# Performance work log

Measured on AMD Instinct MI355X. Metric: run time of the kernel, lower is better.

Reference implementation:

```python
import jax, jax.numpy as jnp
import numpy as np

B, H, W, C = 4, 64, 64, 256
C8 = C // 8

def setup_inputs() -> dict:
    key = jax.random.key(0)
    k1, k2, k3, k4 = jax.random.split(key, 4)
    # glorot-uniform-ish init for 1x1 conv kernels stored as [Cin, Cout]
    def glorot(k, cin, cout):
        lim = np.sqrt(6.0 / (cin + cout)).astype(np.float32)
        return jax.random.uniform(k, (cin, cout), jnp.float32, -lim, lim)
    return {
        "x": jax.random.normal(k1, (B, H, W, C), jnp.float32),
        "kernel_f": glorot(k2, C, C8),
        "kernel_g": glorot(k3, C, C8),
        "kernel_h": glorot(k4, C, C),
        "gamma": jnp.zeros((1,), jnp.float32),
    }

def reference(x, kernel_f, kernel_g, kernel_h, gamma):
    b, h, w, c = x.shape
    n = h * w
    xf = x.reshape(b, n, c)                       # [B, N, C]
    # 1x1 convs == per-position matmuls
    f = jnp.einsum('bnc,cd->bnd', xf, kernel_f)   # [B, N, C/8]
    g = jnp.einsum('bnc,cd->bnd', xf, kernel_g)   # [B, N, C/8]
    hh = jnp.einsum('bnc,cd->bnd', xf, kernel_h)  # [B, N, C]
    s = jnp.einsum('bnd,bmd->bnm', g, f)          # [B, N, N]
    beta = jax.nn.softmax(s, axis=-1)
    o = jnp.einsum('bnm,bmc->bnc', beta, hh)      # [B, N, C]
    o = o.reshape(b, h, w, c)
    return gamma * o + x
```

## Files before the change

### kernel.cpp

```cpp
#include <hip/hip_runtime.h>
#include <hip/hip_bf16.h>

typedef __bf16 bf16x8 __attribute__((ext_vector_type(8)));
typedef float f32x4 __attribute__((ext_vector_type(4)));
typedef float f32x16 __attribute__((ext_vector_type(16)));
typedef unsigned short u16;
typedef unsigned int u32;

__device__ __forceinline__ u16 f2bf_rne(float f){
  union { float f; u32 u; } v; v.f = f;
  u32 r = v.u + 0x7fffu + ((v.u >> 16) & 1u);
  return (u16)(r >> 16);
}
__device__ __forceinline__ u32 pack2(float a, float b){
  return __builtin_amdgcn_perm(__float_as_uint(a), __float_as_uint(b), 0x03020706u);
}
#define BARRIER_LGKM() asm volatile("s_waitcnt lgkmcnt(0)\n\ts_barrier" ::: "memory")

__global__ __launch_bounds__(512) void prep_kernel(
    const float* __restrict__ Wf, const float* __restrict__ Wg,
    const float* __restrict__ Wh, u16* __restrict__ Wfrag){
  const int cc = blockIdx.x;
  const int t = threadIdx.x;
  const int kk = t >> 6, lane = t & 63;
  const int L = lane & 15, quad = lane >> 4;
  const int n = cc * 16 + L;
  u32 pk[4];
  #pragma unroll
  for (int j2 = 0; j2 < 4; ++j2){
    float v[2];
    #pragma unroll
    for (int h = 0; h < 2; ++h){
      int k = kk * 32 + quad * 8 + j2 * 2 + h;
      if (n < 256)      v[h] = Wh[k * 256 + n];
      else if (n < 288) v[h] = Wf[k * 32 + (n - 256)];
      else              v[h] = Wg[k * 32 + (n - 288)];
    }
    pk[j2] = (u32)f2bf_rne(v[0]) | ((u32)f2bf_rne(v[1]) << 16);
  }
  uint4* dst = (uint4*)(Wfrag + ((size_t)(cc * 8 + kk) * 64 + lane) * 8);
  *dst = make_uint4(pk[0], pk[1], pk[2], pk[3]);
}

__global__ __launch_bounds__(512) void proj_kernel(
    const float* __restrict__ x, const u16* __restrict__ Wfrag,
    u16* __restrict__ Qg, u16* __restrict__ Kg, u16* __restrict__ Vfrag)
{
  __shared__ __align__(16) u16 smem[256 * 72];
  u16 (*xb)[264] = (u16(*)[264])smem;
  u16 (*Vr)[72]  = (u16(*)[72])smem;

  const int tid = threadIdx.x;
  const int lane = tid & 63, wave = tid >> 6;
  const int L = lane & 15, quad = lane >> 4;
  const int rowgrp = wave >> 1, colhalf = wave & 1;
  const int n0 = blockIdx.x * 64;

  const float4* xsrc = (const float4*)(x + (size_t)n0 * 256);
  #pragma unroll
  for (int j = 0; j < 8; ++j){
    int idx = j * 512 + tid;
    int row = idx >> 6, col4 = idx & 63;
    float4 v = xsrc[idx];
    u32 p0 = (u32)f2bf_rne(v.x) | ((u32)f2bf_rne(v.y) << 16);
    u32 p1 = (u32)f2bf_rne(v.z) | ((u32)f2bf_rne(v.w) << 16);
    *(uint2*)&xb[row][col4 * 4] = make_uint2(p0, p1);
  }
  __syncthreads();

  f32x4 acc[10];
  #pragma unroll
  for (int cc = 0; cc < 10; ++cc) acc[cc] = (f32x4){0.f, 0.f, 0.f, 0.f};

  #pragma unroll
  for (int kk = 0; kk < 8; ++kk){
    bf16x8 a = *(const bf16x8*)&xb[rowgrp * 16 + L][kk * 32 + quad * 8];
    #pragma unroll
    for (int cc = 0; cc < 10; ++cc){
      int ccg = colhalf * 10 + cc;
      bf16x8 bfr = *(const bf16x8*)(Wfrag + ((size_t)(ccg * 8 + kk) * 64 + lane) * 8);
      acc[cc] = __builtin_amdgcn_mfma_f32_16x16x32_bf16(a, bfr, acc[cc], 0, 0, 0);
    }
  }

  if (colhalf){
    #pragma unroll
    for (int cc = 6; cc < 10; ++cc){
      int ccg = 10 + cc;
      u16* dst = (ccg < 18) ? Kg : Qg;
      float sc = (ccg < 18) ? 1.0f : 1.44269504088896f;
      int c = (ccg & 1) * 16 + L;
      #pragma unroll
      for (int r = 0; r < 4; ++r){
        int row = n0 + rowgrp * 16 + quad * 4 + r;
        dst[(size_t)row * 32 + c] = f2bf_rne(acc[cc][r] * sc);
      }
    }
  }

  __syncthreads();

  {
    const int cmax = colhalf ? 6 : 10;
    for (int cc = 0; cc < cmax; ++cc){
      int ccg = colhalf * 10 + cc;
      int c = ccg * 16 + L;
      #pragma unroll
      for (int r = 0; r < 4; ++r){
        int tn = rowgrp * 16 + quad * 4 + r;
        int p  = ((tn & 15) << 2) | (tn >> 4);
        Vr[c][p] = f2bf_rne(acc[cc][r]);
      }
    }
  }
  __syncthreads();

  u16* Vblk = Vfrag + (size_t)blockIdx.x * (256 * 64);
  #pragma unroll
  for (int i = 0; i < 4; ++i){
    int idx = i * 512 + tid;
    *(uint4*)(Vblk + (size_t)idx * 8) = *(const uint4*)&Vr[idx & 255][(idx >> 8) * 8];
  }
}

__global__ __launch_bounds__(512) void flash_kernel(
    const u16* __restrict__ Qg, const u16* __restrict__ Kg, const u16* __restrict__ Vfrag,
    const float* __restrict__ x, const float* __restrict__ gamma, float* __restrict__ out)
{
  constexpr float SH = -92.33248261689366f;
  __shared__ __align__(16) char smem[73728];
  u16 (*Plds)[2][2][64][72] = (u16 (*)[2][2][64][72])smem;
  float (*Osh)[256] = (float (*)[256])smem;
  __shared__ float Lsh[2][64];

  const int tid = threadIdx.x, lane = tid & 63, wave = tid >> 6;
  const int L = lane & 15, quad = lane >> 4;
  const int m32 = lane & 31, h32 = lane >> 5;
  const int half = wave >> 2, wv = wave & 3;

  const int id = blockIdx.x;
  const int xcd = id & 7;
  const int b = xcd >> 1;
  const int qt = (xcd & 1) * 32 + (id >> 3);
  const int q0 = qt * 64;

  const u16* Qb = Qg + (size_t)(b * 4096) * 32;
  const u16* Kb = Kg + (size_t)(b * 4096) * 32;
  const u16* Vb = Vfrag + (size_t)b * (64 * 256 * 64);
  const float gm = gamma[0];

  const int g0 = half * 32;

  bf16x8 qa = *(const bf16x8*)(Qb + (size_t)(q0 + wv * 16 + L) * 32 + quad * 8);

  const u16* kpA = Kb + (size_t)(g0 * 64 + L) * 32 + quad * 8;
  bf16x8 kcA0 = *(const bf16x8*)(kpA);
  bf16x8 kcA1 = *(const bf16x8*)(kpA + 512);
  bf16x8 kcA2 = *(const bf16x8*)(kpA + 1024);
  bf16x8 kcA3 = *(const bf16x8*)(kpA + 1536);
  const u16* kpB = kpA + 2048;
  bf16x8 kcB0 = *(const bf16x8*)(kpB);
  bf16x8 kcB1 = *(const bf16x8*)(kpB + 512);
  bf16x8 kcB2 = *(const bf16x8*)(kpB + 1024);
  bf16x8 kcB3 = *(const bf16x8*)(kpB + 1536);

  bf16x8 vfA[8], vfB[8];
  {
    const u16* Vt = Vb + (size_t)g0 * (256 * 64);
    #pragma unroll
    for (int ks = 0; ks < 4; ++ks){
      const u16* vrow = Vt + (size_t)((ks * 2 + h32) * 256 + wv * 64 + m32) * 8;
      vfA[ks * 2]     = *(const bf16x8*)(vrow);
      vfA[ks * 2 + 1] = *(const bf16x8*)(vrow + 32 * 8);
      vfB[ks * 2]     = *(const bf16x8*)(vrow + 16384);
      vfB[ks * 2 + 1] = *(const bf16x8*)(vrow + 16384 + 32 * 8);
    }
  }

  f32x16 acc[4];
  #pragma unroll
  for (int t = 0; t < 4; ++t)
    #pragma unroll
    for (int i = 0; i < 16; ++i) acc[t][i] = 0.f;
  float lsum[4] = {0.f, 0.f, 0.f, 0.f};
  const f32x4 zero = (f32x4){0.f, 0.f, 0.f, 0.f};

  for (int it = 0; it < 16; ++it){
    const int g = g0 + it * 2;
    u16 (*PwA)[72] = Plds[half][it & 1][0];
    u16 (*PwB)[72] = Plds[half][it & 1][1];

    f32x4 sA0 = __builtin_amdgcn_mfma_f32_16x16x32_bf16(qa, kcA0, zero, 0, 0, 0);
    f32x4 sA1 = __builtin_amdgcn_mfma_f32_16x16x32_bf16(qa, kcA1, zero, 0, 0, 0);
    f32x4 sA2 = __builtin_amdgcn_mfma_f32_16x16x32_bf16(qa, kcA2, zero, 0, 0, 0);
    f32x4 sA3 = __builtin_amdgcn_mfma_f32_16x16x32_bf16(qa, kcA3, zero, 0, 0, 0);
    f32x4 sB0 = __builtin_amdgcn_mfma_f32_16x16x32_bf16(qa, kcB0, zero, 0, 0, 0);
    f32x4 sB1 = __builtin_amdgcn_mfma_f32_16x16x32_bf16(qa, kcB1, zero, 0, 0, 0);
    f32x4 sB2 = __builtin_amdgcn_mfma_f32_16x16x32_bf16(qa, kcB2, zero, 0, 0, 0);
    f32x4 sB3 = __builtin_amdgcn_mfma_f32_16x16x32_bf16(qa, kcB3, zero, 0, 0, 0);

    if (it < 15){
      const u16* kpa = Kb + (size_t)((g + 2) * 64 + L) * 32 + quad * 8;
      kcA0 = *(const bf16x8*)(kpa);
      kcA1 = *(const bf16x8*)(kpa + 512);
      kcA2 = *(const bf16x8*)(kpa + 1024);
      kcA3 = *(const bf16x8*)(kpa + 1536);
      const u16* kpb = kpa + 2048;
      kcB0 = *(const bf16x8*)(kpb);
      kcB1 = *(const bf16x8*)(kpb + 512);
      kcB2 = *(const bf16x8*)(kpb + 1024);
      kcB3 = *(const bf16x8*)(kpb + 1536);
    }

    #pragma unroll
    for (int r = 0; r < 4; ++r){
      float a0 = __builtin_amdgcn_exp2f(sA0[r] + SH);
      float a1 = __builtin_amdgcn_exp2f(sA1[r] + SH);
      float a2 = __builtin_amdgcn_exp2f(sA2[r] + SH);
      float a3 = __builtin_amdgcn_exp2f(sA3[r] + SH);
      float b0 = __builtin_amdgcn_exp2f(sB0[r] + SH);
      float b1 = __builtin_amdgcn_exp2f(sB1[r] + SH);
      float b2 = __builtin_amdgcn_exp2f(sB2[r] + SH);
      float b3 = __builtin_amdgcn_exp2f(sB3[r] + SH);
      lsum[r] += ((a0 + a1) + (a2 + a3)) + ((b0 + b1) + (b2 + b3));
      *(uint2*)&PwA[wv * 16 + quad * 4 + r][L * 4] =
          make_uint2(pack2(a0, a1), pack2(a2, a3));
      *(uint2*)&PwB[wv * 16 + quad * 4 + r][L * 4] =
          make_uint2(pack2(b0, b1), pack2(b2, b3));
    }

    BARRIER_LGKM();

    #pragma unroll
    for (int ks = 0; ks < 4; ++ks){
      bf16x8 af0 = *(const bf16x8*)&PwA[m32][ks * 16 + h32 * 8];
      bf16x8 af1 = *(const bf16x8*)&PwA[32 + m32][ks * 16 + h32 * 8];
      acc[0] = __builtin_amdgcn_mfma_f32_32x32x16_bf16(af0, vfA[ks*2],   acc[0], 0, 0, 0);
      acc[1] = __builtin_amdgcn_mfma_f32_32x32x16_bf16(af0, vfA[ks*2+1], acc[1], 0, 0, 0);
      acc[2] = __builtin_amdgcn_mfma_f32_32x32x16_bf16(af1, vfA[ks*2],   acc[2], 0, 0, 0);
      acc[3] = __builtin_amdgcn_mfma_f32_32x32x16_bf16(af1, vfA[ks*2+1], acc[3], 0, 0, 0);
    }
    #pragma unroll
    for (int ks = 0; ks < 4; ++ks){
      bf16x8 af0 = *(const bf16x8*)&PwB[m32][ks * 16 + h32 * 8];
      bf16x8 af1 = *(const bf16x8*)&PwB[32 + m32][ks * 16 + h32 * 8];
      acc[0] = __builtin_amdgcn_mfma_f32_32x32x16_bf16(af0, vfB[ks*2],   acc[0], 0, 0, 0);
      acc[1] = __builtin_amdgcn_mfma_f32_32x32x16_bf16(af0, vfB[ks*2+1], acc[1], 0, 0, 0);
      acc[2] = __builtin_amdgcn_mfma_f32_32x32x16_bf16(af1, vfB[ks*2],   acc[2], 0, 0, 0);
      acc[3] = __builtin_amdgcn_mfma_f32_32x32x16_bf16(af1, vfB[ks*2+1], acc[3], 0, 0, 0);
    }

    if (it < 15){
      const u16* Vn = Vb + (size_t)(g + 2) * (256 * 64);
      #pragma unroll
      for (int ks = 0; ks < 4; ++ks){
        const u16* vrow = Vn + (size_t)((ks * 2 + h32) * 256 + wv * 64 + m32) * 8;
        vfA[ks * 2]     = *(const bf16x8*)(vrow);
        vfA[ks * 2 + 1] = *(const bf16x8*)(vrow + 32 * 8);
        vfB[ks * 2]     = *(const bf16x8*)(vrow + 16384);
        vfB[ks * 2 + 1] = *(const bf16x8*)(vrow + 16384 + 32 * 8);
      }
    }
  }

  BARRIER_LGKM();

  #pragma unroll
  for (int r = 0; r < 4; ++r){
    lsum[r] += __shfl_xor(lsum[r], 1);
    lsum[r] += __shfl_xor(lsum[r], 2);
    lsum[r] += __shfl_xor(lsum[r], 4);
    lsum[r] += __shfl_xor(lsum[r], 8);
  }
  if (L == 0){
    #pragma unroll
    for (int r = 0; r < 4; ++r) Lsh[half][wv * 16 + quad * 4 + r] = lsum[r];
  }
  if (half == 1){
    #pragma unroll
    for (int t = 0; t < 4; ++t){
      const int qi = t >> 1, ci = t & 1;
      #pragma unroll
      for (int rg = 0; rg < 16; ++rg){
        int row = qi * 32 + (rg & 3) + 8 * (rg >> 2) + 4 * h32;
        Osh[row][wv * 64 + ci * 32 + m32] = acc[t][rg];
      }
    }
  }
  __syncthreads();
  if (wave == 0){
    float li = gm / (Lsh[0][lane] + Lsh[1][lane]);
    Lsh[0][lane] = li;
  }
  __syncthreads();
  if (half == 0){
    #pragma unroll
    for (int t = 0; t < 4; ++t){
      const int qi = t >> 1, ci = t & 1;
      #pragma unroll
      for (int rg = 0; rg < 16; ++rg){
        int row = qi * 32 + (rg & 3) + 8 * (rg >> 2) + 4 * h32;
        int col = wv * 64 + ci * 32 + m32;
        Osh[row][col] = (acc[t][rg] + Osh[row][col]) * Lsh[0][row];
      }
    }
  }
  __syncthreads();
  const size_t base = ((size_t)(b * 4096) + q0) * 256;
  const float4* xs = (const float4*)(x + base);
  float4* od = (float4*)(out + base);
  const float4* Of = (const float4*)&Osh[0][0];
  #pragma unroll
  for (int i = 0; i < 8; ++i){
    int idx = i * 512 + tid;
    float4 o = Of[idx], xv = xs[idx];
    o.x += xv.x; o.y += xv.y; o.z += xv.z; o.w += xv.w;
    od[idx] = o;
  }
}

extern "C" void kernel_launch(void* const* d_in, const int* in_sizes, int n_in,
                              void* d_out, int out_size, void* d_ws, size_t ws_size,
                              hipStream_t stream) {
  const float* x     = (const float*)d_in[0];
  const float* Wf    = (const float*)d_in[1];
  const float* Wg    = (const float*)d_in[2];
  const float* Wh    = (const float*)d_in[3];
  const float* gamma = (const float*)d_in[4];
  float* out = (float*)d_out;

  u16* p = (u16*)d_ws;
  u16* Qg    = p;  p += 16384 * 32;
  u16* Kg    = p;  p += 16384 * 32;
  u16* Vfrag = p;  p += 4 * 64 * 256 * 64;
  u16* Wfrag = p;  p += 20 * 8 * 64 * 8;

  prep_kernel<<<20, 512, 0, stream>>>(Wf, Wg, Wh, Wfrag);
  proj_kernel<<<256, 512, 0, stream>>>(x, Wfrag, Qg, Kg, Vfrag);
  flash_kernel<<<256, 512, 0, stream>>>(Qg, Kg, Vfrag, x, gamma, out);
}
```

Baseline: 151.7 us.

## Stage K tiles through LDS via async global_load_lds in MFMA fragment layout

```diff
diff --git a/kernel.cpp b/kernel.cpp
--- a/kernel.cpp
+++ b/kernel.cpp
@@ -14,6 +14,10 @@
 }
 __device__ __forceinline__ u32 pack2(float a, float b){
   return __builtin_amdgcn_perm(__float_as_uint(a), __float_as_uint(b), 0x03020706u);
+}
+__device__ __forceinline__ void load_lds16(const void* g, void* l){
+  __builtin_amdgcn_global_load_lds((const __attribute__((address_space(1))) void*)g,
+                                   (__attribute__((address_space(3))) void*)l, 16, 0, 0);
 }
 #define BARRIER_LGKM() asm volatile("s_waitcnt lgkmcnt(0)\n\ts_barrier" ::: "memory")
 
@@ -44,7 +48,7 @@
 
 __global__ __launch_bounds__(512) void proj_kernel(
     const float* __restrict__ x, const u16* __restrict__ Wfrag,
-    u16* __restrict__ Qg, u16* __restrict__ Kg, u16* __restrict__ Vfrag)
+    u16* __restrict__ Qg, u16* __restrict__ Kfrag, u16* __restrict__ Vfrag)
 {
   __shared__ __align__(16) u16 smem[256 * 72];
   u16 (*xb)[264] = (u16(*)[264])smem;
@@ -87,13 +91,17 @@
     #pragma unroll
     for (int cc = 6; cc < 10; ++cc){
       int ccg = 10 + cc;
-      u16* dst = (ccg < 18) ? Kg : Qg;
-      float sc = (ccg < 18) ? 1.0f : 1.44269504088896f;
       int c = (ccg & 1) * 16 + L;
       #pragma unroll
       for (int r = 0; r < 4; ++r){
         int row = n0 + rowgrp * 16 + quad * 4 + r;
-        dst[(size_t)row * 32 + c] = f2bf_rne(acc[cc][r] * sc);
+        if (ccg < 18){
+          size_t off = ((size_t)(row >> 6) * 4 + ((row >> 4) & 3)) * 512
+                     + (c >> 3) * 128 + (row & 15) * 8 + (c & 7);
+          Kfrag[off] = f2bf_rne(acc[cc][r]);
+        } else {
+          Qg[(size_t)row * 32 + c] = f2bf_rne(acc[cc][r] * 1.44269504088896f);
+        }
       }
     }
   }
@@ -124,13 +132,14 @@
 }
 
 __global__ __launch_bounds__(512) void flash_kernel(
-    const u16* __restrict__ Qg, const u16* __restrict__ Kg, const u16* __restrict__ Vfrag,
+    const u16* __restrict__ Qg, const u16* __restrict__ Kfrag, const u16* __restrict__ Vfrag,
     const float* __restrict__ x, const float* __restrict__ gamma, float* __restrict__ out)
 {
   constexpr float SH = -92.33248261689366f;
   __shared__ __align__(16) char smem[73728];
   u16 (*Plds)[2][2][64][72] = (u16 (*)[2][2][64][72])smem;
   float (*Osh)[256] = (float (*)[256])smem;
+  __shared__ __align__(16) u16 Kl[2][2][8][512];
   __shared__ float Lsh[2][64];
 
   const int tid = threadIdx.x, lane = tid & 63, wave = tid >> 6;
@@ -145,25 +154,24 @@
   const int q0 = qt * 64;
 
   const u16* Qb = Qg + (size_t)(b * 4096) * 32;
-  const u16* Kb = Kg + (size_t)(b * 4096) * 32;
+  const u16* Kb = Kfrag + (size_t)b * 131072;
   const u16* Vb = Vfrag + (size_t)b * (64 * 256 * 64);
   const float gm = gamma[0];
 
   const int g0 = half * 32;
+  const int c0 = wv * 2;
 
   bf16x8 qa = *(const bf16x8*)(Qb + (size_t)(q0 + wv * 16 + L) * 32 + quad * 8);
-
-  const u16* kpA = Kb + (size_t)(g0 * 64 + L) * 32 + quad * 8;
-  bf16x8 kcA0 = *(const bf16x8*)(kpA);
-  bf16x8 kcA1 = *(const bf16x8*)(kpA + 512);
-  bf16x8 kcA2 = *(const bf16x8*)(kpA + 1024);
-  bf16x8 kcA3 = *(const bf16x8*)(kpA + 1536);
-  const u16* kpB = kpA + 2048;
-  bf16x8 kcB0 = *(const bf16x8*)(kpB);
-  bf16x8 kcB1 = *(const bf16x8*)(kpB + 512);
-  bf16x8 kcB2 = *(const bf16x8*)(kpB + 1024);
-  bf16x8 kcB3 = *(const bf16x8*)(kpB + 1536);
-
+  asm volatile("" ::: "memory");
+  {
+    const u16* s0 = Kb + ((size_t)(g0 + 0) * 4 + c0) * 512 + lane * 8;
+    load_lds16(s0,       &Kl[half][0][c0][0]);
+    load_lds16(s0 + 512, &Kl[half][0][c0 + 1][0]);
+    const u16* s1 = Kb + ((size_t)(g0 + 2) * 4 + c0) * 512 + lane * 8;
+    load_lds16(s1,       &Kl[half][1][c0][0]);
+    load_lds16(s1 + 512, &Kl[half][1][c0 + 1][0]);
+  }
+  asm volatile("" ::: "memory");
   bf16x8 vfA[8], vfB[8];
   {
     const u16* Vt = Vb + (size_t)g0 * (256 * 64);
@@ -176,6 +184,19 @@
       vfB[ks * 2 + 1] = *(const bf16x8*)(vrow + 16384 + 32 * 8);
     }
   }
+  asm volatile("s_waitcnt vmcnt(18)" ::: "memory");
+  bf16x8 kcA0, kcA1, kcA2, kcA3, kcB0, kcB1, kcB2, kcB3;
+  {
+    const u16 (*Ks)[512] = Kl[half][0];
+    kcA0 = *(const bf16x8*)&Ks[0][lane * 8];
+    kcA1 = *(const bf16x8*)&Ks[1][lane * 8];
+    kcA2 = *(const bf16x8*)&Ks[2][lane * 8];
+    kcA3 = *(const bf16x8*)&Ks[3][lane * 8];
+    kcB0 = *(const bf16x8*)&Ks[4][lane * 8];
+    kcB1 = *(const bf16x8*)&Ks[5][lane * 8];
+    kcB2 = *(const bf16x8*)&Ks[6][lane * 8];
+    kcB3 = *(const bf16x8*)&Ks[7][lane * 8];
+  }
 
   f32x16 acc[4];
   #pragma unroll
@@ -186,7 +207,6 @@
   const f32x4 zero = (f32x4){0.f, 0.f, 0.f, 0.f};
 
   for (int it = 0; it < 16; ++it){
-    const int g = g0 + it * 2;
     u16 (*PwA)[72] = Plds[half][it & 1][0];
     u16 (*PwB)[72] = Plds[half][it & 1][1];
 
@@ -198,19 +218,6 @@
     f32x4 sB1 = __builtin_amdgcn_mfma_f32_16x16x32_bf16(qa, kcB1, zero, 0, 0, 0);
     f32x4 sB2 = __builtin_amdgcn_mfma_f32_16x16x32_bf16(qa, kcB2, zero, 0, 0, 0);
     f32x4 sB3 = __builtin_amdgcn_mfma_f32_16x16x32_bf16(qa, kcB3, zero, 0, 0, 0);
-
-    if (it < 15){
-      const u16* kpa = Kb + (size_t)((g + 2) * 64 + L) * 32 + quad * 8;
-      kcA0 = *(const bf16x8*)(kpa);
-      kcA1 = *(const bf16x8*)(kpa + 512);
-      kcA2 = *(const bf16x8*)(kpa + 1024);
-      kcA3 = *(const bf16x8*)(kpa + 1536);
-      const u16* kpb = kpa + 2048;
-      kcB0 = *(const bf16x8*)(kpb);
-      kcB1 = *(const bf16x8*)(kpb + 512);
-      kcB2 = *(const bf16x8*)(kpb + 1024);
-      kcB3 = *(const bf16x8*)(kpb + 1536);
-    }
 
     #pragma unroll
     for (int r = 0; r < 4; ++r){
@@ -231,6 +238,27 @@
 
     BARRIER_LGKM();
 
+    {
+      int pp = (it + 2) & 15;
+      const u16* ks = Kb + ((size_t)(g0 + pp * 2) * 4 + c0) * 512 + lane * 8;
+      load_lds16(ks,       &Kl[half][it & 1][c0][0]);
+      load_lds16(ks + 512, &Kl[half][it & 1][c0 + 1][0]);
+    }
+    asm volatile("" ::: "memory");
+
+    if (it < 15){
+      asm volatile("s_waitcnt vmcnt(18)" ::: "memory");
+      const u16 (*Ks)[512] = Kl[half][(it + 1) & 1];
+      kcA0 = *(const bf16x8*)&Ks[0][lane * 8];
+      kcA1 = *(const bf16x8*)&Ks[1][lane * 8];
+      kcA2 = *(const bf16x8*)&Ks[2][lane * 8];
+      kcA3 = *(const bf16x8*)&Ks[3][lane * 8];
+      kcB0 = *(const bf16x8*)&Ks[4][lane * 8];
+      kcB1 = *(const bf16x8*)&Ks[5][lane * 8];
+      kcB2 = *(const bf16x8*)&Ks[6][lane * 8];
+      kcB3 = *(const bf16x8*)&Ks[7][lane * 8];
+    }
+
     #pragma unroll
     for (int ks = 0; ks < 4; ++ks){
       bf16x8 af0 = *(const bf16x8*)&PwA[m32][ks * 16 + h32 * 8];
@@ -251,7 +279,7 @@
     }
 
     if (it < 15){
-      const u16* Vn = Vb + (size_t)(g + 2) * (256 * 64);
+      const u16* Vn = Vb + (size_t)(g0 + (it + 1) * 2) * (256 * 64);
       #pragma unroll
       for (int ks = 0; ks < 4; ++ks){
         const u16* vrow = Vn + (size_t)((ks * 2 + h32) * 256 + wv * 64 + m32) * 8;
@@ -331,11 +359,11 @@
 
   u16* p = (u16*)d_ws;
   u16* Qg    = p;  p += 16384 * 32;
-  u16* Kg    = p;  p += 16384 * 32;
+  u16* Kfrag = p;  p += 256 * 4 * 64 * 8;
   u16* Vfrag = p;  p += 4 * 64 * 256 * 64;
   u16* Wfrag = p;  p += 20 * 8 * 64 * 8;
 
   prep_kernel<<<20, 512, 0, stream>>>(Wf, Wg, Wh, Wfrag);
-  proj_kernel<<<256, 512, 0, stream>>>(x, Wfrag, Qg, Kg, Vfrag);
-  flash_kernel<<<256, 512, 0, stream>>>(Qg, Kg, Vfrag, x, gamma, out);
-}
+  proj_kernel<<<256, 512, 0, stream>>>(x, Wfrag, Qg, Kfrag, Vfrag);
+  flash_kernel<<<256, 512, 0, stream>>>(Qg, Kfrag, Vfrag, x, gamma, out);
+}
```

After: 153.0 us. About the same (+0.9%).

## Warp-specialize flash kernel into QK/softmax producer and PV consumer waves

Applied to the files above, without the earlier changes.

```diff
diff --git a/kernel.cpp b/kernel.cpp
--- a/kernel.cpp
+++ b/kernel.cpp
@@ -128,15 +128,16 @@
     const float* __restrict__ x, const float* __restrict__ gamma, float* __restrict__ out)
 {
   constexpr float SH = -92.33248261689366f;
-  __shared__ __align__(16) char smem[73728];
-  u16 (*Plds)[2][2][64][72] = (u16 (*)[2][2][64][72])smem;
+  __shared__ __align__(16) char smem[65536];
+  u16 (*Plds)[2][64][72] = (u16 (*)[2][64][72])smem;
   float (*Osh)[256] = (float (*)[256])smem;
-  __shared__ float Lsh[2][64];
+  __shared__ float Lsh[64];
 
   const int tid = threadIdx.x, lane = tid & 63, wave = tid >> 6;
   const int L = lane & 15, quad = lane >> 4;
   const int m32 = lane & 31, h32 = lane >> 5;
-  const int half = wave >> 2, wv = wave & 3;
+  const bool producer = wave < 4;
+  const int pw = wave & 3;
 
   const int id = blockIdx.x;
   const int xcd = id & 7;
@@ -149,27 +150,25 @@
   const u16* Vb = Vfrag + (size_t)b * (64 * 256 * 64);
   const float gm = gamma[0];
 
-  const int g0 = half * 32;
-
-  bf16x8 qa = *(const bf16x8*)(Qb + (size_t)(q0 + wv * 16 + L) * 32 + quad * 8);
-
-  const u16* kpA = Kb + (size_t)(g0 * 64 + L) * 32 + quad * 8;
-  bf16x8 kcA0 = *(const bf16x8*)(kpA);
-  bf16x8 kcA1 = *(const bf16x8*)(kpA + 512);
-  bf16x8 kcA2 = *(const bf16x8*)(kpA + 1024);
-  bf16x8 kcA3 = *(const bf16x8*)(kpA + 1536);
-  const u16* kpB = kpA + 2048;
-  bf16x8 kcB0 = *(const bf16x8*)(kpB);
-  bf16x8 kcB1 = *(const bf16x8*)(kpB + 512);
-  bf16x8 kcB2 = *(const bf16x8*)(kpB + 1024);
-  bf16x8 kcB3 = *(const bf16x8*)(kpB + 1536);
-
+  bf16x8 qa;
+  bf16x8 kcA0, kcA1, kcA2, kcA3, kcB0, kcB1, kcB2, kcB3;
   bf16x8 vfA[8], vfB[8];
-  {
-    const u16* Vt = Vb + (size_t)g0 * (256 * 64);
+  if (producer){
+    qa = *(const bf16x8*)(Qb + (size_t)(q0 + pw * 16 + L) * 32 + quad * 8);
+    const u16* kpA = Kb + (size_t)(0 * 64 + L) * 32 + quad * 8;
+    kcA0 = *(const bf16x8*)(kpA);
+    kcA1 = *(const bf16x8*)(kpA + 512);
+    kcA2 = *(const bf16x8*)(kpA + 1024);
+    kcA3 = *(const bf16x8*)(kpA + 1536);
+    const u16* kpB = kpA + 2048;
+    kcB0 = *(const bf16x8*)(kpB);
+    kcB1 = *(const bf16x8*)(kpB + 512);
+    kcB2 = *(const bf16x8*)(kpB + 1024);
+    kcB3 = *(const bf16x8*)(kpB + 1536);
+  } else {
     #pragma unroll
     for (int ks = 0; ks < 4; ++ks){
-      const u16* vrow = Vt + (size_t)((ks * 2 + h32) * 256 + wv * 64 + m32) * 8;
+      const u16* vrow = Vb + (size_t)((ks * 2 + h32) * 256 + pw * 64 + m32) * 8;
       vfA[ks * 2]     = *(const bf16x8*)(vrow);
       vfA[ks * 2 + 1] = *(const bf16x8*)(vrow + 32 * 8);
       vfB[ks * 2]     = *(const bf16x8*)(vrow + 16384);
@@ -185,126 +184,113 @@
   float lsum[4] = {0.f, 0.f, 0.f, 0.f};
   const f32x4 zero = (f32x4){0.f, 0.f, 0.f, 0.f};
 
-  for (int it = 0; it < 16; ++it){
-    const int g = g0 + it * 2;
-    u16 (*PwA)[72] = Plds[half][it & 1][0];
-    u16 (*PwB)[72] = Plds[half][it & 1][1];
-
-    f32x4 sA0 = __builtin_amdgcn_mfma_f32_16x16x32_bf16(qa, kcA0, zero, 0, 0, 0);
-    f32x4 sA1 = __builtin_amdgcn_mfma_f32_16x16x32_bf16(qa, kcA1, zero, 0, 0, 0);
-    f32x4 sA2 = __builtin_amdgcn_mfma_f32_16x16x32_bf16(qa, kcA2, zero, 0, 0, 0);
-    f32x4 sA3 = __builtin_amdgcn_mfma_f32_16x16x32_bf16(qa, kcA3, zero, 0, 0, 0);
-    f32x4 sB0 = __builtin_amdgcn_mfma_f32_16x16x32_bf16(qa, kcB0, zero, 0, 0, 0);
-    f32x4 sB1 = __builtin_amdgcn_mfma_f32_16x16x32_bf16(qa, kcB1, zero, 0, 0, 0);
-    f32x4 sB2 = __builtin_amdgcn_mfma_f32_16x16x32_bf16(qa, kcB2, zero, 0, 0, 0);
-    f32x4 sB3 = __builtin_amdgcn_mfma_f32_16x16x32_bf16(qa, kcB3, zero, 0, 0, 0);
-
-    if (it < 15){
-      const u16* kpa = Kb + (size_t)((g + 2) * 64 + L) * 32 + quad * 8;
-      kcA0 = *(const bf16x8*)(kpa);
-      kcA1 = *(const bf16x8*)(kpa + 512);
-      kcA2 = *(const bf16x8*)(kpa + 1024);
-      kcA3 = *(const bf16x8*)(kpa + 1536);
-      const u16* kpb = kpa + 2048;
-      kcB0 = *(const bf16x8*)(kpb);
-      kcB1 = *(const bf16x8*)(kpb + 512);
-      kcB2 = *(const bf16x8*)(kpb + 1024);
-      kcB3 = *(const bf16x8*)(kpb + 1536);
-    }
-
+  for (int it = 0; it < 32; ++it){
+    u16 (*PwA)[72] = Plds[it & 1][0];
+    u16 (*PwB)[72] = Plds[it & 1][1];
+
+    if (producer){
+      f32x4 sA0 = __builtin_amdgcn_mfma_f32_16x16x32_bf16(qa, kcA0, zero, 0, 0, 0);
+      f32x4 sA1 = __builtin_amdgcn_mfma_f32_16x16x32_bf16(qa, kcA1, zero, 0, 0, 0);
+      f32x4 sA2 = __builtin_amdgcn_mfma_f32_16x16x32_bf16(qa, kcA2, zero, 0, 0, 0);
+      f32x4 sA3 = __builtin_amdgcn_mfma_f32_16x16x32_bf16(qa, kcA3, zero, 0, 0, 0);
+      f32x4 sB0 = __builtin_amdgcn_mfma_f32_16x16x32_bf16(qa, kcB0, zero, 0, 0, 0);
+      f32x4 sB1 = __builtin_amdgcn_mfma_f32_16x16x32_bf16(qa, kcB1, zero, 0, 0, 0);
+      f32x4 sB2 = __builtin_amdgcn_mfma_f32_16x16x32_bf16(qa, kcB2, zero, 0, 0, 0);
+      f32x4 sB3 = __builtin_amdgcn_mfma_f32_16x16x32_bf16(qa, kcB3, zero, 0, 0, 0);
+
+      if (it < 31){
+        const u16* kpa = Kb + (size_t)((2 * it + 2) * 64 + L) * 32 + quad * 8;
+        kcA0 = *(const bf16x8*)(kpa);
+        kcA1 = *(const bf16x8*)(kpa + 512);
+        kcA2 = *(const bf16x8*)(kpa + 1024);
+        kcA3 = *(const bf16x8*)(kpa + 1536);
+        const u16* kpb = kpa + 2048;
+        kcB0 = *(const bf16x8*)(kpb);
+        kcB1 = *(const bf16x8*)(kpb + 512);
+        kcB2 = *(const bf16x8*)(kpb + 1024);
+        kcB3 = *(const bf16x8*)(kpb + 1536);
+      }
+
+      #pragma unroll
+      for (int r = 0; r < 4; ++r){
+        float a0 = __builtin_amdgcn_exp2f(sA0[r] + SH);
+        float a1 = __builtin_amdgcn_exp2f(sA1[r] + SH);
+        float a2 = __builtin_amdgcn_exp2f(sA2[r] + SH);
+        float a3 = __builtin_amdgcn_exp2f(sA3[r] + SH);
+        float b0 = __builtin_amdgcn_exp2f(sB0[r] + SH);
+        float b1 = __builtin_amdgcn_exp2f(sB1[r] + SH);
+        float b2 = __builtin_amdgcn_exp2f(sB2[r] + SH);
+        float b3 = __builtin_amdgcn_exp2f(sB3[r] + SH);
+        lsum[r] += ((a0 + a1) + (a2 + a3)) + ((b0 + b1) + (b2 + b3));
+        *(uint2*)&PwA[pw * 16 + quad * 4 + r][L * 4] =
+            make_uint2(pack2(a0, a1), pack2(a2, a3));
+        *(uint2*)&PwB[pw * 16 + quad * 4 + r][L * 4] =
+            make_uint2(pack2(b0, b1), pack2(b2, b3));
+      }
+    }
+
+    BARRIER_LGKM();
+
+    if (!producer){
+      #pragma unroll
+      for (int ks = 0; ks < 4; ++ks){
+        bf16x8 af0 = *(const bf16x8*)&PwA[m32][ks * 16 + h32 * 8];
+        bf16x8 af1 = *(const bf16x8*)&PwA[32 + m32][ks * 16 + h32 * 8];
+        acc[0] = __builtin_amdgcn_mfma_f32_32x32x16_bf16(af0, vfA[ks*2],   acc[0], 0, 0, 0);
+        acc[1] = __builtin_amdgcn_mfma_f32_32x32x16_bf16(af0, vfA[ks*2+1], acc[1], 0, 0, 0);
+        acc[2] = __builtin_amdgcn_mfma_f32_32x32x16_bf16(af1, vfA[ks*2],   acc[2], 0, 0, 0);
+        acc[3] = __builtin_amdgcn_mfma_f32_32x32x16_bf16(af1, vfA[ks*2+1], acc[3], 0, 0, 0);
+      }
+      #pragma unroll
+      for (int ks = 0; ks < 4; ++ks){
+        bf16x8 af0 = *(const bf16x8*)&PwB[m32][ks * 16 + h32 * 8];
+        bf16x8 af1 = *(const bf16x8*)&PwB[32 + m32][ks * 16 + h32 * 8];
+        acc[0] = __builtin_amdgcn_mfma_f32_32x32x16_bf16(af0, vfB[ks*2],   acc[0], 0, 0, 0);
+        acc[1] = __builtin_amdgcn_mfma_f32_32x32x16_bf16(af0, vfB[ks*2+1], acc[1], 0, 0, 0);
+        acc[2] = __builtin_amdgcn_mfma_f32_32x32x16_bf16(af1, vfB[ks*2],   acc[2], 0, 0, 0);
+        acc[3] = __builtin_amdgcn_mfma_f32_32x32x16_bf16(af1, vfB[ks*2+1], acc[3], 0, 0, 0);
+      }
+      if (it < 31){
+        const u16* Vn = Vb + (size_t)(2 * it + 2) * (256 * 64);
+        #pragma unroll
+        for (int ks = 0; ks < 4; ++ks){
+          const u16* vrow = Vn + (size_t)((ks * 2 + h32) * 256 + pw * 64 + m32) * 8;
+          vfA[ks * 2]     = *(const bf16x8*)(vrow);
+          vfA[ks * 2 + 1] = *(const bf16x8*)(vrow + 32 * 8);
+          vfB[ks * 2]     = *(const bf16x8*)(vrow + 16384);
+          vfB[ks * 2 + 1] = *(const bf16x8*)(vrow + 16384 + 32 * 8);
+        }
+      }
+    }
+  }
+
+  BARRIER_LGKM();
+
+  if (producer){
     #pragma unroll
     for (int r = 0; r < 4; ++r){
-      float a0 = __builtin_amdgcn_exp2f(sA0[r] + SH);
-      float a1 = __builtin_amdgcn_exp2f(sA1[r] + SH);
-      float a2 = __builtin_amdgcn_exp2f(sA2[r] + SH);
-      float a3 = __builtin_amdgcn_exp2f(sA3[r] + SH);
-      float b0 = __builtin_amdgcn_exp2f(sB0[r] + SH);
-      float b1 = __builtin_amdgcn_exp2f(sB1[r] + SH);
-      float b2 = __builtin_amdgcn_exp2f(sB2[r] + SH);
-      float b3 = __builtin_amdgcn_exp2f(sB3[r] + SH);
-      lsum[r] += ((a0 + a1) + (a2 + a3)) + ((b0 + b1) + (b2 + b3));
-      *(uint2*)&PwA[wv * 16 + quad * 4 + r][L * 4] =
-          make_uint2(pack2(a0, a1), pack2(a2, a3));
-      *(uint2*)&PwB[wv * 16 + quad * 4 + r][L * 4] =
-          make_uint2(pack2(b0, b1), pack2(b2, b3));
-    }
-
-    BARRIER_LGKM();
-
-    #pragma unroll
-    for (int ks = 0; ks < 4; ++ks){
-      bf16x8 af0 = *(const bf16x8*)&PwA[m32][ks * 16 + h32 * 8];
-      bf16x8 af1 = *(const bf16x8*)&PwA[32 + m32][ks * 16 + h32 * 8];
-      acc[0] = __builtin_amdgcn_mfma_f32_32x32x16_bf16(af0, vfA[ks*2],   acc[0], 0, 0, 0);
-      acc[1] = __builtin_amdgcn_mfma_f32_32x32x16_bf16(af0, vfA[ks*2+1], acc[1], 0, 0, 0);
-      acc[2] = __builtin_amdgcn_mfma_f32_32x32x16_bf16(af1, vfA[ks*2],   acc[2], 0, 0, 0);
-      acc[3] = __builtin_amdgcn_mfma_f32_32x32x16_bf16(af1, vfA[ks*2+1], acc[3], 0, 0, 0);
-    }
-    #pragma unroll
-    for (int ks = 0; ks < 4; ++ks){
-      bf16x8 af0 = *(const bf16x8*)&PwB[m32][ks * 16 + h32 * 8];
-      bf16x8 af1 = *(const bf16x8*)&PwB[32 + m32][ks * 16 + h32 * 8];
-      acc[0] = __builtin_amdgcn_mfma_f32_32x32x16_bf16(af0, vfB[ks*2],   acc[0], 0, 0, 0);
-      acc[1] = __builtin_amdgcn_mfma_f32_32x32x16_bf16(af0, vfB[ks*2+1], acc[1], 0, 0, 0);
-      acc[2] = __builtin_amdgcn_mfma_f32_32x32x16_bf16(af1, vfB[ks*2],   acc[2], 0, 0, 0);
-      acc[3] = __builtin_amdgcn_mfma_f32_32x32x16_bf16(af1, vfB[ks*2+1], acc[3], 0, 0, 0);
-    }
-
-    if (it < 15){
-      const u16* Vn = Vb + (size_t)(g + 2) * (256 * 64);
-      #pragma unroll
-      for (int ks = 0; ks < 4; ++ks){
-        const u16* vrow = Vn + (size_t)((ks * 2 + h32) * 256 + wv * 64 + m32) * 8;
-        vfA[ks * 2]     = *(const bf16x8*)(vrow);
-        vfA[ks * 2 + 1] = *(const bf16x8*)(vrow + 32 * 8);
-        vfB[ks * 2]     = *(const bf16x8*)(vrow + 16384);
-        vfB[ks * 2 + 1] = *(const bf16x8*)(vrow + 16384 + 32 * 8);
-      }
-    }
-  }
-
-  BARRIER_LGKM();
-
-  #pragma unroll
-  for (int r = 0; r < 4; ++r){
-    lsum[r] += __shfl_xor(lsum[r], 1);
-    lsum[r] += __shfl_xor(lsum[r], 2);
-    lsum[r] += __shfl_xor(lsum[r], 4);
-    lsum[r] += __shfl_xor(lsum[r], 8);
-  }
-  if (L == 0){
-    #pragma unroll
-    for (int r = 0; r < 4; ++r) Lsh[half][wv * 16 + quad * 4 + r] = lsum[r];
-  }
-  if (half == 1){
+      lsum[r] += __shfl_xor(lsum[r], 1);
+      lsum[r] += __shfl_xor(lsum[r], 2);
+      lsum[r] += __shfl_xor(lsum[r], 4);
+      lsum[r] += __shfl_xor(lsum[r], 8);
+    }
+    if (L == 0){
+      #pragma unroll
+      for (int r = 0; r < 4; ++r) Lsh[pw * 16 + quad * 4 + r] = lsum[r];
+    }
+  } else {
     #pragma unroll
     for (int t = 0; t < 4; ++t){
       const int qi = t >> 1, ci = t & 1;
       #pragma unroll
       for (int rg = 0; rg < 16; ++rg){
         int row = qi * 32 + (rg & 3) + 8 * (rg >> 2) + 4 * h32;
-        Osh[row][wv * 64 + ci * 32 + m32] = acc[t][rg];
-      }
-    }
-  }
-  __syncthreads();
-  if (wave == 0){
-    float li = gm / (Lsh[0][lane] + Lsh[1][lane]);
-    Lsh[0][lane] = li;
-  }
-  __syncthreads();
-  if (half == 0){
-    #pragma unroll
-    for (int t = 0; t < 4; ++t){
-      const int qi = t >> 1, ci = t & 1;
-      #pragma unroll
-      for (int rg = 0; rg < 16; ++rg){
-        int row = qi * 32 + (rg & 3) + 8 * (rg >> 2) + 4 * h32;
-        int col = wv * 64 + ci * 32 + m32;
-        Osh[row][col] = (acc[t][rg] + Osh[row][col]) * Lsh[0][row];
-      }
-    }
-  }
+        Osh[row][pw * 64 + ci * 32 + m32] = acc[t][rg];
+      }
+    }
+  }
+  __syncthreads();
+  if (wave == 0) Lsh[lane] = gm / Lsh[lane];
   __syncthreads();
   const size_t base = ((size_t)(b * 4096) + q0) * 256;
   const float4* xs = (const float4*)(x + base);
@@ -313,8 +299,10 @@
   #pragma unroll
   for (int i = 0; i < 8; ++i){
     int idx = i * 512 + tid;
+    float li = Lsh[idx >> 6];
     float4 o = Of[idx], xv = xs[idx];
-    o.x += xv.x; o.y += xv.y; o.z += xv.z; o.w += xv.w;
+    o.x = o.x * li + xv.x; o.y = o.y * li + xv.y;
+    o.z = o.z * li + xv.z; o.w = o.w * li + xv.w;
     od[idx] = o;
   }
 }
```

New measurement: 148.7 us. About the same (-2.0%).
